# Kernel optimization log

Measured on AMD Instinct MI355X. Metric: run time of the kernel, lower is better.

Reference implementation:

```python
import jax, jax.numpy as jnp
import numpy as np
from jax.experimental.jet import jet

ORDER = 3  # Taylor order from init_kwargs
D, C, H = 4096, 4096, 8192


def setup_inputs() -> dict:
    key = jax.random.key(0)
    k = jax.random.split(key, 6)
    sc1 = 1.0 / np.sqrt(D + C)
    sc2 = 1.0 / np.sqrt(H)
    return {
        "h": jax.random.normal(k[0], (D,), jnp.float32),
        "r": jnp.zeros((), jnp.float32),  # ignored residual slot of h_r tuple
        "t": jax.random.uniform(k[1], (), jnp.float32),
        "c": jax.random.normal(k[2], (C,), jnp.float32),
        "W1": jax.random.normal(k[3], (D + C, H), jnp.float32) * sc1,
        "b1": jnp.zeros((H,), jnp.float32),
        "W2": jax.random.normal(k[4], (H, D), jnp.float32) * sc2,
        "b2": jnp.zeros((D,), jnp.float32),
    }


def reference(h, r, t, c, W1, b1, W2, b2):
    # dynamics f(h, t, c): 2-layer tanh MLP on concat(h, c)
    def f(_h, _t, _c):
        x = jnp.concatenate((_h, _c))
        return jnp.tanh(x @ W1 + b1) @ W2 + b2

    h_shape = h.shape

    def g(h_t):
        # expand flattened state+time through dynamics
        _h, _t = jnp.reshape(h_t[:-1], h_shape), h_t[-1]
        dh = jnp.ravel(f(_h, _t, c))
        return jnp.concatenate((dh, jnp.array([1.0], dtype=dh.dtype)))

    h_t = jnp.concatenate((jnp.ravel(h), jnp.reshape(t, (1,))))
    # recursive Taylor-mode jet expansion
    (y0, [*yns]) = jet(g, (h_t,), ((jnp.ones_like(h_t),),))
    for _ in range(ORDER - 1):
        (y0, [*yns]) = jet(g, (h_t,), ((y0, *yns),))
    dydt = jnp.reshape(y0[:-1], h_shape)
    drdt = jnp.reshape(yns[-2][:-1], h_shape)
    return (dydt, jnp.mean(drdt ** 2))
```

## Files before the change

kernel.cpp:

```cpp
#include <hip/hip_runtime.h>

#define DD 4096
#define HH 8192

enum Stage { S_X0 = 0, S_TANH, S_BIASOUT, S_PMUL, S_COPY, S_S2 };

typedef float vfloat4 __attribute__((ext_vector_type(4)));

__device__ inline unsigned short f2bf(float f) {
    unsigned int u = __float_as_uint(f);
    u += 0x7FFFu + ((u >> 16) & 1u);
    return (unsigned short)(u >> 16);
}

template <bool NT, bool CONV, int KS, int NTOT>
__device__ inline void stream_f32(const float* __restrict__ Wp,
                                  const float* __restrict__ xs,
                                  float* __restrict__ op,
                                  unsigned short* __restrict__ Wbp) {
    float ax = 0.f, ay = 0.f, az = 0.f, aw = 0.f;
#pragma unroll 8
    for (int k = 0; k < KS; ++k) {
        const float xv = xs[k];
        const float* row = Wp + (size_t)k * NTOT;
        vfloat4 w;
        if constexpr (NT)
            w = __builtin_nontemporal_load(reinterpret_cast<const vfloat4*>(row));
        else
            w = *reinterpret_cast<const vfloat4*>(row);
        ax = fmaf(xv, w.x, ax);
        ay = fmaf(xv, w.y, ay);
        az = fmaf(xv, w.z, az);
        aw = fmaf(xv, w.w, aw);
        if constexpr (CONV) {
            ushort4 o;
            o.x = f2bf(w.x); o.y = f2bf(w.y); o.z = f2bf(w.z); o.w = f2bf(w.w);
            *reinterpret_cast<ushort4*>(Wbp + (size_t)k * NTOT) = o;
        }
    }
    *reinterpret_cast<float4*>(op) = make_float4(ax, ay, az, aw);
}

template <int STAGE, int KS, int SPREV, int KPREV>
__device__ inline void prologue(const float* __restrict__ Pprev,
                                const float* __restrict__ h, const float* __restrict__ c,
                                const float* __restrict__ b1, const float* __restrict__ b2,
                                float* __restrict__ s0g, float* __restrict__ t0g,
                                float* __restrict__ a1g, float* __restrict__ outv,
                                float* xs, float* part, int k0, int bx)
{
    constexpr int GROUPS = 256 / KS;
    const int tid = threadIdx.x;
    if constexpr (STAGE == S_X0) {
        if (tid < KS) {
            int k = k0 + tid;
            xs[tid] = (k < DD) ? h[k] : c[k - DD];
        }
    } else {
        const int g = tid / KS, j = tid % KS;
        float acc = 0.f;
        for (int s = g; s < SPREV; s += GROUPS)
            acc += Pprev[(size_t)s * KPREV + k0 + j];
        part[g * KS + j] = acc;
        __syncthreads();
        if (tid < KS) {
            const int k = k0 + tid;
            float tot = 0.f;
#pragma unroll
            for (int g2 = 0; g2 < GROUPS; ++g2) tot += part[g2 * KS + tid];
            float xv;
            if constexpr (STAGE == S_TANH) {
                float s = tanhf(tot + b1[k]);
                xv = s;
                if (bx == 0) { s0g[k] = s; t0g[k] = 1.f - s * s; }
            } else if constexpr (STAGE == S_BIASOUT) {
                xv = tot + b2[k];
                if (bx == 0) outv[k] = xv;
            } else if constexpr (STAGE == S_PMUL) {
                xv = t0g[k] * tot;
                if (bx == 0) a1g[k] = tot;
            } else if constexpr (STAGE == S_COPY) {
                xv = tot;
            } else {
                float a1v = a1g[k];
                xv = t0g[k] * (tot - s0g[k] * a1v * a1v);
            }
            xs[tid] = xv;
        }
    }
    __syncthreads();
}

template <int STAGE, int KS, int SPREV, int KPREV, int NTOT, int NTMODE, bool CONV>
__global__ __launch_bounds__(256) void gemv_f32(
    const float* __restrict__ W, const float* __restrict__ Pprev,
    float* __restrict__ Pout, unsigned short* __restrict__ Wb,
    const float* __restrict__ h, const float* __restrict__ c,
    const float* __restrict__ b1, const float* __restrict__ b2,
    float* __restrict__ s0g, float* __restrict__ t0g, float* __restrict__ a1g,
    float* __restrict__ outv)
{
    __shared__ float xs[KS];
    __shared__ float part[256];
    const int bx = blockIdx.x, by = blockIdx.y;
    const int k0 = by * KS;
    prologue<STAGE, KS, SPREV, KPREV>(Pprev, h, c, b1, b2, s0g, t0g, a1g, outv,
                                      xs, part, k0, bx);

    const int ncol = bx * 1024 + threadIdx.x * 4;
    const float* Wp = W + (size_t)k0 * NTOT + ncol;
    float* op = Pout + (size_t)by * NTOT + ncol;
    unsigned short* Wbp = CONV ? (Wb + (size_t)k0 * NTOT + ncol) : nullptr;

    if constexpr (NTMODE == 0) {
        stream_f32<false, false, KS, NTOT>(Wp, xs, op, nullptr);
    } else if constexpr (NTMODE == 1) {
        stream_f32<true, false, KS, NTOT>(Wp, xs, op, nullptr);
    } else {
        if (k0 >= DD) stream_f32<true, false, KS, NTOT>(Wp, xs, op, nullptr);
        else          stream_f32<false, CONV, KS, NTOT>(Wp, xs, op, Wbp);
    }
}

template <int STAGE, int KS, int SPREV, int KPREV, int NTOT>
__global__ __launch_bounds__(256) void gemv_b16(
    const unsigned short* __restrict__ Wb, const float* __restrict__ Pprev,
    float* __restrict__ Pout,
    const float* __restrict__ h, const float* __restrict__ c,
    const float* __restrict__ b1, const float* __restrict__ b2,
    float* __restrict__ s0g, float* __restrict__ t0g, float* __restrict__ a1g,
    float* __restrict__ outv)
{
    __shared__ float xs[KS];
    __shared__ float part[256];
    const int bx = blockIdx.x, by = blockIdx.y;
    const int k0 = by * KS;
    prologue<STAGE, KS, SPREV, KPREV>(Pprev, h, c, b1, b2, s0g, t0g, a1g, outv,
                                      xs, part, k0, bx);

    const int ncol = bx * 2048 + threadIdx.x * 8;
    const unsigned short* Wp = Wb + (size_t)k0 * NTOT + ncol;
    float a0 = 0.f, a1 = 0.f, a2 = 0.f, a3 = 0.f;
    float a4 = 0.f, a5 = 0.f, a6 = 0.f, a7 = 0.f;
#pragma unroll 8
    for (int k = 0; k < KS; ++k) {
        const float xv = xs[k];
        const uint4 w = *reinterpret_cast<const uint4*>(Wp + (size_t)k * NTOT);
        a0 = fmaf(xv, __uint_as_float(w.x << 16), a0);
        a1 = fmaf(xv, __uint_as_float(w.x & 0xFFFF0000u), a1);
        a2 = fmaf(xv, __uint_as_float(w.y << 16), a2);
        a3 = fmaf(xv, __uint_as_float(w.y & 0xFFFF0000u), a3);
        a4 = fmaf(xv, __uint_as_float(w.z << 16), a4);
        a5 = fmaf(xv, __uint_as_float(w.z & 0xFFFF0000u), a5);
        a6 = fmaf(xv, __uint_as_float(w.w << 16), a6);
        a7 = fmaf(xv, __uint_as_float(w.w & 0xFFFF0000u), a7);
    }
    float* op = Pout + (size_t)by * NTOT + ncol;
    *reinterpret_cast<float4*>(op)     = make_float4(a0, a1, a2, a3);
    *reinterpret_cast<float4*>(op + 4) = make_float4(a4, a5, a6, a7);
}

template <int SPREV>
__global__ __launch_bounds__(256) void reduce_sq_partial(const float* __restrict__ P6,
                                                         float* __restrict__ partial) {
    const int n = blockIdx.x * 256 + threadIdx.x;
    float acc = 0.f;
#pragma unroll 8
    for (int s = 0; s < SPREV; ++s) acc += P6[(size_t)s * DD + n];
    float sq = acc * acc;
    for (int off = 32; off; off >>= 1) sq += __shfl_down(sq, off);
    __shared__ float ls[4];
    const int wid = threadIdx.x >> 6;
    if ((threadIdx.x & 63) == 0) ls[wid] = sq;
    __syncthreads();
    if (threadIdx.x == 0) partial[blockIdx.x] = ls[0] + ls[1] + ls[2] + ls[3];
}

__global__ __launch_bounds__(64) void finalize_meansq(const float* __restrict__ partial,
                                                      float* __restrict__ dout) {
    float v = (threadIdx.x < 16) ? partial[threadIdx.x] : 0.f;
    for (int off = 8; off; off >>= 1) v += __shfl_down(v, off);
    if (threadIdx.x == 0) dout[DD] = v / (float)DD;
}

extern "C" void kernel_launch(void* const* d_in, const int* in_sizes, int n_in,
                              void* d_out, int out_size, void* d_ws, size_t ws_size,
                              hipStream_t stream) {
    const float* h  = (const float*)d_in[0];
    const float* c  = (const float*)d_in[3];
    const float* W1 = (const float*)d_in[4];
    const float* b1 = (const float*)d_in[5];
    const float* W2 = (const float*)d_in[6];
    const float* b2 = (const float*)d_in[7];
    float* out = (float*)d_out;
    float* ws = (float*)d_ws;

    float* P1 = ws;
    float* P2 = P1 + 1048576;
    float* P3 = P2 + 1048576;
    float* P4 = P3 + 2097152;
    float* P5 = P4 + 1048576;
    float* P6 = P5 + 2097152;
    float* s0 = P6 + 1048576;
    float* t0 = s0 + 8192;
    float* a1 = t0 + 8192;
    float* psum = a1 + 8192;
    unsigned short* W1b = (unsigned short*)(psum + 64);

    gemv_f32<S_X0, 64, 1, 1, HH, 2, true><<<dim3(8, 128), 256, 0, stream>>>(
        W1, nullptr, P1, W1b, h, c, b1, b2, s0, t0, a1, out);
    gemv_f32<S_TANH, 32, 128, HH, DD, 0, false><<<dim3(4, 256), 256, 0, stream>>>(
        W2, P1, P2, nullptr, h, c, b1, b2, s0, t0, a1, out);
    gemv_b16<S_BIASOUT, 16, 256, DD, HH><<<dim3(4, 256), 256, 0, stream>>>(
        W1b, P2, P3, h, c, b1, b2, s0, t0, a1, out);
    gemv_f32<S_PMUL, 32, 256, HH, DD, 0, false><<<dim3(4, 256), 256, 0, stream>>>(
        W2, P3, P4, nullptr, h, c, b1, b2, s0, t0, a1, out);
    gemv_b16<S_COPY, 16, 256, DD, HH><<<dim3(4, 256), 256, 0, stream>>>(
        W1b, P4, P5, h, c, b1, b2, s0, t0, a1, out);
    gemv_f32<S_S2, 32, 256, HH, DD, 1, false><<<dim3(4, 256), 256, 0, stream>>>(
        W2, P5, P6, nullptr, h, c, b1, b2, s0, t0, a1, out);
    reduce_sq_partial<256><<<16, 256, 0, stream>>>(P6, psum);
    finalize_meansq<<<1, 64, 0, stream>>>(psum, out);
}
```

Baseline: 202.8 us.

## Convert W2 to bf16 on first pass and reuse for later W2 GEMVs

The first W2 GEMV now also writes a bf16 copy of W2 into workspace, and the later two W2 GEMVs (PMUL and S2 stages) read that bf16 copy instead of re-streaming the fp32 weights. This halves weight bytes for those passes, which are bandwidth bound. All fp32 loads are now nontemporal. The cost is an extra 64MB write in the first W2 pass, a changed partial-sum layout (512 K-splits), and reduced precision in the higher-order Taylor terms.

Result: slower. 220.1 us (+8.6%).

```diff
diff --git a/kernel.cpp b/kernel.cpp
--- a/kernel.cpp
+++ b/kernel.cpp
@@ -11,34 +11,6 @@
     unsigned int u = __float_as_uint(f);
     u += 0x7FFFu + ((u >> 16) & 1u);
     return (unsigned short)(u >> 16);
-}
-
-template <bool NT, bool CONV, int KS, int NTOT>
-__device__ inline void stream_f32(const float* __restrict__ Wp,
-                                  const float* __restrict__ xs,
-                                  float* __restrict__ op,
-                                  unsigned short* __restrict__ Wbp) {
-    float ax = 0.f, ay = 0.f, az = 0.f, aw = 0.f;
-#pragma unroll 8
-    for (int k = 0; k < KS; ++k) {
-        const float xv = xs[k];
-        const float* row = Wp + (size_t)k * NTOT;
-        vfloat4 w;
-        if constexpr (NT)
-            w = __builtin_nontemporal_load(reinterpret_cast<const vfloat4*>(row));
-        else
-            w = *reinterpret_cast<const vfloat4*>(row);
-        ax = fmaf(xv, w.x, ax);
-        ay = fmaf(xv, w.y, ay);
-        az = fmaf(xv, w.z, az);
-        aw = fmaf(xv, w.w, aw);
-        if constexpr (CONV) {
-            ushort4 o;
-            o.x = f2bf(w.x); o.y = f2bf(w.y); o.z = f2bf(w.z); o.w = f2bf(w.w);
-            *reinterpret_cast<ushort4*>(Wbp + (size_t)k * NTOT) = o;
-        }
-    }
-    *reinterpret_cast<float4*>(op) = make_float4(ax, ay, az, aw);
 }
 
 template <int STAGE, int KS, int SPREV, int KPREV>
@@ -91,7 +63,7 @@
     __syncthreads();
 }
 
-template <int STAGE, int KS, int SPREV, int KPREV, int NTOT, int NTMODE, bool CONV>
+template <int STAGE, int KS, int SPREV, int KPREV, int NTOT, int CONVROWS>
 __global__ __launch_bounds__(256) void gemv_f32(
     const float* __restrict__ W, const float* __restrict__ Pprev,
     float* __restrict__ Pout, unsigned short* __restrict__ Wb,
@@ -110,16 +82,26 @@
     const int ncol = bx * 1024 + threadIdx.x * 4;
     const float* Wp = W + (size_t)k0 * NTOT + ncol;
     float* op = Pout + (size_t)by * NTOT + ncol;
-    unsigned short* Wbp = CONV ? (Wb + (size_t)k0 * NTOT + ncol) : nullptr;
-
-    if constexpr (NTMODE == 0) {
-        stream_f32<false, false, KS, NTOT>(Wp, xs, op, nullptr);
-    } else if constexpr (NTMODE == 1) {
-        stream_f32<true, false, KS, NTOT>(Wp, xs, op, nullptr);
-    } else {
-        if (k0 >= DD) stream_f32<true, false, KS, NTOT>(Wp, xs, op, nullptr);
-        else          stream_f32<false, CONV, KS, NTOT>(Wp, xs, op, Wbp);
+    unsigned short* Wbp = Wb + (size_t)k0 * NTOT + ncol;
+    const bool doConv = (k0 < CONVROWS);
+
+    float ax = 0.f, ay = 0.f, az = 0.f, aw = 0.f;
+#pragma unroll 8
+    for (int k = 0; k < KS; ++k) {
+        const float xv = xs[k];
+        const float* row = Wp + (size_t)k * NTOT;
+        vfloat4 w = __builtin_nontemporal_load(reinterpret_cast<const vfloat4*>(row));
+        ax = fmaf(xv, w.x, ax);
+        ay = fmaf(xv, w.y, ay);
+        az = fmaf(xv, w.z, az);
+        aw = fmaf(xv, w.w, aw);
+        if (doConv) {
+            ushort4 o;
+            o.x = f2bf(w.x); o.y = f2bf(w.y); o.z = f2bf(w.z); o.w = f2bf(w.w);
+            *reinterpret_cast<ushort4*>(Wbp + (size_t)k * NTOT) = o;
+        }
     }
+    *reinterpret_cast<float4*>(op) = make_float4(ax, ay, az, aw);
 }
 
 template <int STAGE, int KS, int SPREV, int KPREV, int NTOT>
@@ -199,26 +181,27 @@
     float* P2 = P1 + 1048576;
     float* P3 = P2 + 1048576;
     float* P4 = P3 + 2097152;
-    float* P5 = P4 + 1048576;
+    float* P5 = P4 + 2097152;
     float* P6 = P5 + 2097152;
-    float* s0 = P6 + 1048576;
+    float* s0 = P6 + 2097152;
     float* t0 = s0 + 8192;
     float* a1 = t0 + 8192;
     float* psum = a1 + 8192;
     unsigned short* W1b = (unsigned short*)(psum + 64);
-
-    gemv_f32<S_X0, 64, 1, 1, HH, 2, true><<<dim3(8, 128), 256, 0, stream>>>(
+    unsigned short* W2b = W1b + (size_t)DD * HH;
+
+    gemv_f32<S_X0, 64, 1, 1, HH, DD><<<dim3(8, 128), 256, 0, stream>>>(
         W1, nullptr, P1, W1b, h, c, b1, b2, s0, t0, a1, out);
-    gemv_f32<S_TANH, 32, 128, HH, DD, 0, false><<<dim3(4, 256), 256, 0, stream>>>(
-        W2, P1, P2, nullptr, h, c, b1, b2, s0, t0, a1, out);
+    gemv_f32<S_TANH, 32, 128, HH, DD, HH><<<dim3(4, 256), 256, 0, stream>>>(
+        W2, P1, P2, W2b, h, c, b1, b2, s0, t0, a1, out);
     gemv_b16<S_BIASOUT, 16, 256, DD, HH><<<dim3(4, 256), 256, 0, stream>>>(
         W1b, P2, P3, h, c, b1, b2, s0, t0, a1, out);
-    gemv_f32<S_PMUL, 32, 256, HH, DD, 0, false><<<dim3(4, 256), 256, 0, stream>>>(
-        W2, P3, P4, nullptr, h, c, b1, b2, s0, t0, a1, out);
-    gemv_b16<S_COPY, 16, 256, DD, HH><<<dim3(4, 256), 256, 0, stream>>>(
+    gemv_b16<S_PMUL, 16, 256, HH, DD><<<dim3(2, 512), 256, 0, stream>>>(
+        W2b, P3, P4, h, c, b1, b2, s0, t0, a1, out);
+    gemv_b16<S_COPY, 16, 512, DD, HH><<<dim3(4, 256), 256, 0, stream>>>(
         W1b, P4, P5, h, c, b1, b2, s0, t0, a1, out);
-    gemv_f32<S_S2, 32, 256, HH, DD, 1, false><<<dim3(4, 256), 256, 0, stream>>>(
-        W2, P5, P6, nullptr, h, c, b1, b2, s0, t0, a1, out);
-    reduce_sq_partial<256><<<16, 256, 0, stream>>>(P6, psum);
+    gemv_b16<S_S2, 16, 256, HH, DD><<<dim3(2, 512), 256, 0, stream>>>(
+        W2b, P5, P6, h, c, b1, b2, s0, t0, a1, out);
+    reduce_sq_partial<512><<<16, 256, 0, stream>>>(P6, psum);
     finalize_meansq<<<1, 64, 0, stream>>>(psum, out);
 }
```
